# Kernel tuning notes

Measured on AMD Instinct MI355X. Metric: run time of the kernel, lower is better.

## Reference

```python
import jax, jax.numpy as jnp
import numpy as np

D_IN = 1024
D_OUT = 1024
CTX_LEN = 2048
BATCH = 4
SEQ = 2048


def setup_inputs() -> dict:
    key = jax.random.key(0)
    kx, kq, kk, kv = jax.random.split(key, 4)
    x = jax.random.normal(kx, (BATCH, SEQ, D_IN), dtype=jnp.float32)
    s = 1.0 / np.sqrt(D_IN)
    # torch nn.Linear weight is (d_out, d_in); store transposed for x @ W
    W_q = jax.random.uniform(kq, (D_IN, D_OUT), dtype=jnp.float32, minval=-s, maxval=s)
    W_k = jax.random.uniform(kk, (D_IN, D_OUT), dtype=jnp.float32, minval=-s, maxval=s)
    W_v = jax.random.uniform(kv, (D_IN, D_OUT), dtype=jnp.float32, minval=-s, maxval=s)
    return {"x": x, "W_q": W_q, "W_k": W_k, "W_v": W_v}


def reference(x, W_q, W_k, W_v):
    b, n, _ = x.shape
    d_out = W_q.shape[1]
    q = x @ W_q            # [b, n, d_out]
    k = x @ W_k
    v = x @ W_v
    scores = jnp.einsum('bqd,bkd->bqk', q, k)  # [b, n, n]
    causal = jnp.triu(jnp.ones((n, n), dtype=bool), k=1)
    scores = jnp.where(causal, -jnp.inf, scores)
    attn = jax.nn.softmax(scores / jnp.sqrt(jnp.float32(d_out)), axis=-1)
    # dropout p=0.0 -> identity
    return jnp.einsum('bqk,bkd->bqd', attn, v)
```

## Files before the change

kernel.cpp:

```cpp
#include <hip/hip_runtime.h>
#include <hip/hip_bf16.h>

#define BATCH 4
#define SEQ   2048
#define DIN   1024
#define DOUT  1024
#define N3    3072
#define MTOT  (BATCH*SEQ)

typedef __hip_bfloat16 bf16;
typedef __attribute__((ext_vector_type(8))) short bf16x8;
typedef __attribute__((ext_vector_type(4))) float f32x4;

#define MFMA(a,b,c) __builtin_amdgcn_mfma_f32_16x16x32_bf16(a,b,c,0,0,0)

union pack4 { bf16 h[4]; uint2 u2; };
union pack8 { bf16 h[8]; bf16x8 v; };

__device__ __forceinline__ void gl16(const bf16* g, bf16* l)
{
    __builtin_amdgcn_global_load_lds(
        (const __attribute__((address_space(1))) void*)g,
        (__attribute__((address_space(3))) void*)l, 16, 0, 0);
}


__global__ __launch_bounds__(256)
void k_prep(const float* __restrict__ x, const float* __restrict__ Wq,
            const float* __restrict__ Wk, const float* __restrict__ Wv,
            bf16* __restrict__ xb, bf16* __restrict__ Wt)
{
    __shared__ bf16 t[64][68];
    const int bid = blockIdx.x;
    if (bid < 8192) {
        long i = ((long)bid * 256 + threadIdx.x) * 4;
        float4 v = *(const float4*)(x + i);
        pack4 o;
        o.h[0] = __float2bfloat16(v.x);
        o.h[1] = __float2bfloat16(v.y);
        o.h[2] = __float2bfloat16(v.z);
        o.h[3] = __float2bfloat16(v.w);
        *(uint2*)(xb + i) = o.u2;
        return;
    }
    const int idx = bid - 8192;
    const int mat = idx >> 8;
    const int rem = idx & 255;
    const int k0 = (rem >> 4) * 64, n0 = (rem & 15) * 64;
    const float* W = (mat == 0) ? Wq : ((mat == 1) ? Wk : Wv);
#pragma unroll
    for (int p = 0; p < 4; ++p) {
        int kr = p * 16 + (threadIdx.x >> 4);
        int c4 = (threadIdx.x & 15) * 4;
        float4 v = *(const float4*)&W[(long)(k0 + kr) * DOUT + n0 + c4];
        t[c4 + 0][kr] = __float2bfloat16(v.x);
        t[c4 + 1][kr] = __float2bfloat16(v.y);
        t[c4 + 2][kr] = __float2bfloat16(v.z);
        t[c4 + 3][kr] = __float2bfloat16(v.w);
    }
    __syncthreads();
    bf16* O = Wt + (long)mat * DIN * DOUT;
#pragma unroll
    for (int i = 0; i < 2; ++i) {
        int l = threadIdx.x + i * 256;
        int n = l >> 3, c8 = (l & 7) * 8;
        pack8 o;
#pragma unroll
        for (int j = 0; j < 8; ++j) o.h[j] = t[n][c8 + j];
        *(bf16x8*)&O[(long)(n0 + n) * DIN + k0 + c8] = o.v;
    }
}


__device__ __forceinline__ void gemm_core(
    const bf16* __restrict__ Ab, long lda,
    const bf16* __restrict__ Bb, long ldb,
    int nk, bf16* __restrict__ As, bf16* __restrict__ Bs,
    f32x4 acc[4][4])
{
    const int tid  = threadIdx.x;
    const int lane = tid & 63;
    const int wave = tid >> 6;
    const int wm = (wave >> 1) * 64;
    const int wn = (wave & 1) * 64;
    const int r  = lane & 15;
    const int qd = lane >> 4;

    const int row0 = tid >> 3;
    const int c    = (tid & 7) ^ (row0 & 7);
    const long aoff = (long)row0 * lda + c * 8;
    const long boff = (long)row0 * ldb + c * 8;
    const long astep = 32 * lda, bstep = 32 * ldb;
    bf16* dA = &As[tid * 8];
    bf16* dB = &Bs[tid * 8];

    for (int kk = 0; kk < nk; ++kk) {
        const bf16* A = Ab + kk * 64 + aoff;
        const bf16* B = Bb + kk * 64 + boff;
#pragma unroll
        for (int i = 0; i < 4; ++i) {
            gl16(A + i * astep, dA + i * 2048);
            gl16(B + i * bstep, dB + i * 2048);
        }
        __syncthreads();
#pragma unroll
        for (int ks = 0; ks < 2; ++ks) {
            const int slot = ((ks * 4 + qd) ^ (r & 7)) * 8;
            bf16x8 af[4], bv[4];
#pragma unroll
            for (int mi = 0; mi < 4; ++mi)
                af[mi] = *(const bf16x8*)&As[(wm + mi * 16 + r) * 64 + slot];
#pragma unroll
            for (int ni = 0; ni < 4; ++ni)
                bv[ni] = *(const bf16x8*)&Bs[(wn + ni * 16 + r) * 64 + slot];
#pragma unroll
            for (int mi = 0; mi < 4; ++mi)
#pragma unroll
                for (int ni = 0; ni < 4; ++ni)
                    acc[mi][ni] = MFMA(af[mi], bv[ni], acc[mi][ni]);
        }
        __syncthreads();
    }
}


__global__ __launch_bounds__(256)
void k_gemm_qkv(const bf16* __restrict__ xb, const bf16* __restrict__ Wt,
                bf16* __restrict__ QK, bf16* __restrict__ Vt)
{
    __shared__ __align__(16) bf16 smem[17408];
    bf16* As = smem;
    bf16* Bs = smem + 8192;
    const int m0 = blockIdx.y * 128, n0 = blockIdx.x * 128;
    f32x4 acc[4][4] = {};
    gemm_core(xb + (long)m0 * DIN, DIN, Wt + (long)n0 * DIN, DIN, DIN / 64, As, Bs, acc);

    const int tid = threadIdx.x;
    const int lane = tid & 63, wave = tid >> 6;
    const int wm = (wave >> 1) * 64, wn = (wave & 1) * 64;
    const int r = lane & 15, qd = lane >> 4;

    if (n0 < 2048) {
#pragma unroll
        for (int mi = 0; mi < 4; ++mi)
#pragma unroll
            for (int ni = 0; ni < 4; ++ni)
#pragma unroll
                for (int j = 0; j < 4; ++j) {
                    int row = m0 + wm + mi * 16 + qd * 4 + j;
                    int col = n0 + wn + ni * 16 + r;
                    QK[(long)row * 2048 + col] = __float2bfloat16(acc[mi][ni][j]);
                }
    } else {
        const int ld = 136;
        bf16* T = smem;
#pragma unroll
        for (int mi = 0; mi < 4; ++mi)
#pragma unroll
            for (int ni = 0; ni < 4; ++ni) {
                pack4 p;
#pragma unroll
                for (int j = 0; j < 4; ++j) p.h[j] = __float2bfloat16(acc[mi][ni][j]);
                int d_l = wn + ni * 16 + r;
                int s_l = wm + mi * 16 + qd * 4;
                *(uint2*)&T[d_l * ld + s_l] = p.u2;
            }
        __syncthreads();
        const int n0v = n0 - 2048;
        const int bb = m0 >> 11;
        const int s0 = m0 & 2047;
        bf16* Ob = Vt + (long)bb * DOUT * SEQ + s0;
#pragma unroll
        for (int p = 0; p < 8; ++p) {
            int l = tid + p * 256;
            int d = l >> 4, s8 = (l & 15) * 8;
            bf16x8 vv = *(const bf16x8*)&T[d * ld + s8];
            *(bf16x8*)&Ob[(long)(n0v + d) * SEQ + s8] = vv;
        }
    }
}


__global__ __launch_bounds__(256, 3)
void k_gemm_scores(const bf16* __restrict__ QK, bf16* __restrict__ P,
                   float* __restrict__ rowSum)
{
    const int b = blockIdx.z, qt = blockIdx.y, kt = blockIdx.x;
    if (kt > qt) return;
    __shared__ __align__(16) bf16 As[128 * 64];
    __shared__ __align__(16) bf16 Bs[128 * 64];
    const bf16* A  = QK + (long)b * SEQ * 2048;
    const bf16* Bt = A + 1024;
    f32x4 acc[4][4] = {};
    gemm_core(A + (long)qt * 128 * 2048, 2048, Bt + (long)kt * 128 * 2048, 2048,
              DIN / 64, As, Bs, acc);

    bf16* Pb = P + (long)b * SEQ * SEQ;
    float* RS = rowSum + b * SEQ;
    const int lane = threadIdx.x & 63, wave = threadIdx.x >> 6;
    const int wm = (wave >> 1) * 64, wn = (wave & 1) * 64;
    const int r = lane & 15, qd = lane >> 4;

    float rp[4][4];
#pragma unroll
    for (int mi = 0; mi < 4; ++mi)
#pragma unroll
        for (int j = 0; j < 4; ++j) rp[mi][j] = 0.f;

#pragma unroll
    for (int mi = 0; mi < 4; ++mi)
#pragma unroll
        for (int ni = 0; ni < 4; ++ni)
#pragma unroll
            for (int j = 0; j < 4; ++j) {
                int row = qt * 128 + wm + mi * 16 + qd * 4 + j;
                int col = kt * 128 + wn + ni * 16 + r;
                float e = (col > row) ? 0.f : __expf(acc[mi][ni][j] * 0.03125f);
                rp[mi][j] += e;
                Pb[(long)row * SEQ + col] = __float2bfloat16(e);
            }
#pragma unroll
    for (int d = 1; d < 16; d <<= 1)
#pragma unroll
        for (int mi = 0; mi < 4; ++mi)
#pragma unroll
            for (int j = 0; j < 4; ++j)
                rp[mi][j] += __shfl_xor(rp[mi][j], d, 64);
    if (r == 0) {
#pragma unroll
        for (int mi = 0; mi < 4; ++mi)
#pragma unroll
            for (int j = 0; j < 4; ++j) {
                int row = qt * 128 + wm + mi * 16 + qd * 4 + j;
                atomicAdd(&RS[row], rp[mi][j]);
            }
    }
}


__global__ __launch_bounds__(256, 3)
void k_gemm_pv(const bf16* __restrict__ P, const bf16* __restrict__ Vt,
               const float* __restrict__ rowSum, float* __restrict__ O)
{
    const int b = blockIdx.z, nt = blockIdx.x;
    const int qt = (SEQ / 128 - 1) - blockIdx.y;
    __shared__ __align__(16) bf16 As[128 * 64];
    __shared__ __align__(16) bf16 Bs[128 * 64];
    const bf16* A  = P + (long)b * SEQ * SEQ + (long)qt * 128 * SEQ;
    const bf16* Bt = Vt + (long)b * DOUT * SEQ;
    const int nk = (qt + 1) * 2;
    f32x4 acc[4][4] = {};
    gemm_core(A, SEQ, Bt + (long)nt * 128 * SEQ, SEQ, nk, As, Bs, acc);

    float* Ob = O + (long)b * SEQ * DOUT;
    const float* RS = rowSum + b * SEQ;
    const int lane = threadIdx.x & 63, wave = threadIdx.x >> 6;
    const int wm = (wave >> 1) * 64, wn = (wave & 1) * 64;
    const int r = lane & 15, qd = lane >> 4;
#pragma unroll
    for (int mi = 0; mi < 4; ++mi)
#pragma unroll
        for (int j = 0; j < 4; ++j) {
            int row = qt * 128 + wm + mi * 16 + qd * 4 + j;
            float inv = 1.0f / RS[row];
#pragma unroll
            for (int ni = 0; ni < 4; ++ni) {
                int col = nt * 128 + wn + ni * 16 + r;
                Ob[(long)row * DOUT + col] = acc[mi][ni][j] * inv;
            }
        }
}


extern "C" void kernel_launch(void* const* d_in, const int* in_sizes, int n_in,
                              void* d_out, int out_size, void* d_ws, size_t ws_size,
                              hipStream_t stream)
{
    const float* x  = (const float*)d_in[0];
    const float* Wq = (const float*)d_in[1];
    const float* Wk = (const float*)d_in[2];
    const float* Wv = (const float*)d_in[3];
    float* out = (float*)d_out;

    char* ws = (char*)d_ws;
    bf16*  xb = (bf16*)(ws);
    bf16*  Wt = (bf16*)(ws + 16777216);
    bf16*  QK = (bf16*)(ws + 23068672);
    bf16*  Vt = (bf16*)(ws + 56623104);
    bf16*  P  = (bf16*)(ws + 73400320);
    float* RS = (float*)(ws + 106954752);

    hipMemsetAsync(RS, 0, BATCH * SEQ * sizeof(float), stream);
    k_prep<<<dim3(8192 + 768), 256, 0, stream>>>(x, Wq, Wk, Wv, xb, Wt);
    k_gemm_qkv<<<dim3(N3 / 128, MTOT / 128), 256, 0, stream>>>(xb, Wt, QK, Vt);
    k_gemm_scores<<<dim3(SEQ / 128, SEQ / 128, BATCH), 256, 0, stream>>>(QK, P, RS);
    k_gemm_pv<<<dim3(DOUT / 128, SEQ / 128, BATCH), 256, 0, stream>>>(P, Vt, RS, out);
}
```

Before: 225.1 us.

## Stage GEMM epilogues through LDS for coalesced stores; compact causal score grid

The QK, scores and PV epilogues now write their accumulator tiles into shared memory and then emit 16-byte coalesced global stores, replacing scattered 2-byte and 4-byte per-element stores. The PV kernel stages its fp32 output in two 64-row halves so the tile fits in the existing LDS buffer. The scores kernel launches only the 136 lower-triangular tiles per batch, recovering the (qt,kt) pair with a sqrt-based index, so no blocks launch only to exit early. The cost is extra LDS traffic and barriers in each epilogue.

```diff
diff --git a/kernel.cpp b/kernel.cpp
--- a/kernel.cpp
+++ b/kernel.cpp
@@ -139,6 +139,8 @@
     const int lane = tid & 63, wave = tid >> 6;
     const int wm = (wave >> 1) * 64, wn = (wave & 1) * 64;
     const int r = lane & 15, qd = lane >> 4;
+    const int ld = 136;
+    bf16* T = smem;
 
     if (n0 < 2048) {
 #pragma unroll
@@ -146,14 +148,18 @@
 #pragma unroll
             for (int ni = 0; ni < 4; ++ni)
 #pragma unroll
-                for (int j = 0; j < 4; ++j) {
-                    int row = m0 + wm + mi * 16 + qd * 4 + j;
-                    int col = n0 + wn + ni * 16 + r;
-                    QK[(long)row * 2048 + col] = __float2bfloat16(acc[mi][ni][j]);
-                }
+                for (int j = 0; j < 4; ++j)
+                    T[(wm + mi * 16 + qd * 4 + j) * ld + wn + ni * 16 + r] =
+                        __float2bfloat16(acc[mi][ni][j]);
+        __syncthreads();
+#pragma unroll
+        for (int i = 0; i < 8; ++i) {
+            int l = tid + i * 256;
+            int rr = l >> 4, c8 = (l & 15) * 8;
+            bf16x8 v = *(const bf16x8*)&T[rr * ld + c8];
+            *(bf16x8*)&QK[(long)(m0 + rr) * 2048 + n0 + c8] = v;
+        }
     } else {
-        const int ld = 136;
-        bf16* T = smem;
 #pragma unroll
         for (int mi = 0; mi < 4; ++mi)
 #pragma unroll
@@ -185,10 +191,16 @@
 void k_gemm_scores(const bf16* __restrict__ QK, bf16* __restrict__ P,
                    float* __restrict__ rowSum)
 {
-    const int b = blockIdx.z, qt = blockIdx.y, kt = blockIdx.x;
-    if (kt > qt) return;
-    __shared__ __align__(16) bf16 As[128 * 64];
-    __shared__ __align__(16) bf16 Bs[128 * 64];
+    const int b = blockIdx.z;
+    int i = blockIdx.x;
+    int qt = (int)((sqrtf(8.f * i + 1.f) - 1.f) * 0.5f);
+    if (qt * (qt + 1) / 2 > i) --qt;
+    else if ((qt + 1) * (qt + 2) / 2 <= i) ++qt;
+    const int kt = i - qt * (qt + 1) / 2;
+
+    __shared__ __align__(16) bf16 smem[17408];
+    bf16* As = smem;
+    bf16* Bs = smem + 8192;
     const bf16* A  = QK + (long)b * SEQ * 2048;
     const bf16* Bt = A + 1024;
     f32x4 acc[4][4] = {};
@@ -197,9 +209,12 @@
 
     bf16* Pb = P + (long)b * SEQ * SEQ;
     float* RS = rowSum + b * SEQ;
-    const int lane = threadIdx.x & 63, wave = threadIdx.x >> 6;
+    const int tid = threadIdx.x;
+    const int lane = tid & 63, wave = tid >> 6;
     const int wm = (wave >> 1) * 64, wn = (wave & 1) * 64;
     const int r = lane & 15, qd = lane >> 4;
+    const int ld = 136;
+    bf16* T = smem;
 
     float rp[4][4];
 #pragma unroll
@@ -213,12 +228,21 @@
         for (int ni = 0; ni < 4; ++ni)
 #pragma unroll
             for (int j = 0; j < 4; ++j) {
-                int row = qt * 128 + wm + mi * 16 + qd * 4 + j;
-                int col = kt * 128 + wn + ni * 16 + r;
-                float e = (col > row) ? 0.f : __expf(acc[mi][ni][j] * 0.03125f);
+                int row_l = wm + mi * 16 + qd * 4 + j;
+                int col_l = wn + ni * 16 + r;
+                float e = (kt * 128 + col_l > qt * 128 + row_l)
+                          ? 0.f : __expf(acc[mi][ni][j] * 0.03125f);
                 rp[mi][j] += e;
-                Pb[(long)row * SEQ + col] = __float2bfloat16(e);
+                T[row_l * ld + col_l] = __float2bfloat16(e);
             }
+    __syncthreads();
+#pragma unroll
+    for (int i2 = 0; i2 < 8; ++i2) {
+        int l = tid + i2 * 256;
+        int rr = l >> 4, c8 = (l & 15) * 8;
+        bf16x8 v = *(const bf16x8*)&T[rr * ld + c8];
+        *(bf16x8*)&Pb[(long)(qt * 128 + rr) * SEQ + kt * 128 + c8] = v;
+    }
 #pragma unroll
     for (int d = 1; d < 16; d <<= 1)
 #pragma unroll
@@ -244,8 +268,9 @@
 {
     const int b = blockIdx.z, nt = blockIdx.x;
     const int qt = (SEQ / 128 - 1) - blockIdx.y;
-    __shared__ __align__(16) bf16 As[128 * 64];
-    __shared__ __align__(16) bf16 Bs[128 * 64];
+    __shared__ __align__(16) bf16 smem[17408];
+    bf16* As = smem;
+    bf16* Bs = smem + 8192;
     const bf16* A  = P + (long)b * SEQ * SEQ + (long)qt * 128 * SEQ;
     const bf16* Bt = Vt + (long)b * DOUT * SEQ;
     const int nk = (qt + 1) * 2;
@@ -254,21 +279,37 @@
 
     float* Ob = O + (long)b * SEQ * DOUT;
     const float* RS = rowSum + b * SEQ;
-    const int lane = threadIdx.x & 63, wave = threadIdx.x >> 6;
-    const int wm = (wave >> 1) * 64, wn = (wave & 1) * 64;
+    const int tid = threadIdx.x;
+    const int lane = tid & 63, wave = tid >> 6;
+    const int wn = (wave & 1) * 64;
     const int r = lane & 15, qd = lane >> 4;
-#pragma unroll
-    for (int mi = 0; mi < 4; ++mi)
-#pragma unroll
-        for (int j = 0; j < 4; ++j) {
-            int row = qt * 128 + wm + mi * 16 + qd * 4 + j;
-            float inv = 1.0f / RS[row];
-#pragma unroll
-            for (int ni = 0; ni < 4; ++ni) {
-                int col = nt * 128 + wn + ni * 16 + r;
-                Ob[(long)row * DOUT + col] = acc[mi][ni][j] * inv;
-            }
-        }
+    const int ldf = 132;
+    float* T = (float*)smem;
+
+#pragma unroll
+    for (int h = 0; h < 2; ++h) {
+        if ((wave >> 1) == h) {
+#pragma unroll
+            for (int mi = 0; mi < 4; ++mi)
+#pragma unroll
+                for (int j = 0; j < 4; ++j) {
+                    int row_l = mi * 16 + qd * 4 + j;
+                    float inv = 1.0f / RS[qt * 128 + h * 64 + row_l];
+#pragma unroll
+                    for (int ni = 0; ni < 4; ++ni)
+                        T[row_l * ldf + wn + ni * 16 + r] = acc[mi][ni][j] * inv;
+                }
+        }
+        __syncthreads();
+#pragma unroll
+        for (int i = 0; i < 8; ++i) {
+            int l = tid + i * 256;
+            int rr = l >> 5, c4 = (l & 31) * 4;
+            float4 v = *(const float4*)&T[rr * ldf + c4];
+            *(float4*)&Ob[(long)(qt * 128 + h * 64 + rr) * DOUT + nt * 128 + c4] = v;
+        }
+        __syncthreads();
+    }
 }
 
 
@@ -293,6 +334,6 @@
     hipMemsetAsync(RS, 0, BATCH * SEQ * sizeof(float), stream);
     k_prep<<<dim3(8192 + 768), 256, 0, stream>>>(x, Wq, Wk, Wv, xb, Wt);
     k_gemm_qkv<<<dim3(N3 / 128, MTOT / 128), 256, 0, stream>>>(xb, Wt, QK, Vt);
-    k_gemm_scores<<<dim3(SEQ / 128, SEQ / 128, BATCH), 256, 0, stream>>>(QK, P, RS);
+    k_gemm_scores<<<dim3(136, 1, BATCH), 256, 0, stream>>>(QK, P, RS);
     k_gemm_pv<<<dim3(DOUT / 128, SEQ / 128, BATCH), 256, 0, stream>>>(P, Vt, RS, out);
 }
```

Measured after the change: 232.9 us. 3.5% more time.

## Double-buffer LDS in attention GEMMs, compact causal grid, stage QK stores via LDS

Applied to the files above, without the earlier changes.

Adds a double-buffered GEMM core that prefetches the next K-slice into a second LDS buffer while MFMAs run on the current one. The scores and PV kernels use it, with occupancy hints lowered to 2 blocks because LDS per block doubles. The scores launch now covers only the 136 lower-triangular tiles per batch, decoding (qt, kt) with a sqrt, so no blocks launch just to exit. The QKV epilogue stages Q/K tiles through LDS so global writes are 16-byte vectors instead of scattered 2-byte stores.

```diff
diff --git a/kernel.cpp b/kernel.cpp
--- a/kernel.cpp
+++ b/kernel.cpp
@@ -124,6 +124,72 @@
 }
 
 
+__device__ __forceinline__ void gemm_core_db(
+    const bf16* __restrict__ Ab, long lda,
+    const bf16* __restrict__ Bb, long ldb,
+    int nk, bf16* __restrict__ As, bf16* __restrict__ Bs,
+    f32x4 acc[4][4])
+{
+    const int tid  = threadIdx.x;
+    const int lane = tid & 63;
+    const int wave = tid >> 6;
+    const int wm = (wave >> 1) * 64;
+    const int wn = (wave & 1) * 64;
+    const int r  = lane & 15;
+    const int qd = lane >> 4;
+
+    const int row0 = tid >> 3;
+    const int c    = (tid & 7) ^ (row0 & 7);
+    const long aoff = (long)row0 * lda + c * 8;
+    const long boff = (long)row0 * ldb + c * 8;
+    const long astep = 32 * lda, bstep = 32 * ldb;
+
+    {
+        const bf16* A = Ab + aoff;
+        const bf16* B = Bb + boff;
+        bf16* dA = &As[tid * 8];
+        bf16* dB = &Bs[tid * 8];
+#pragma unroll
+        for (int i = 0; i < 4; ++i) {
+            gl16(A + i * astep, dA + i * 2048);
+            gl16(B + i * bstep, dB + i * 2048);
+        }
+    }
+    for (int kk = 0; kk < nk; ++kk) {
+        __syncthreads();
+        const int cur = (kk & 1) * 8192;
+        if (kk + 1 < nk) {
+            const int nxt = 8192 - cur;
+            const bf16* A = Ab + (kk + 1) * 64 + aoff;
+            const bf16* B = Bb + (kk + 1) * 64 + boff;
+            bf16* dA = &As[nxt + tid * 8];
+            bf16* dB = &Bs[nxt + tid * 8];
+#pragma unroll
+            for (int i = 0; i < 4; ++i) {
+                gl16(A + i * astep, dA + i * 2048);
+                gl16(B + i * bstep, dB + i * 2048);
+            }
+        }
+#pragma unroll
+        for (int ks = 0; ks < 2; ++ks) {
+            const int slot = ((ks * 4 + qd) ^ (r & 7)) * 8;
+            bf16x8 af[4], bv[4];
+#pragma unroll
+            for (int mi = 0; mi < 4; ++mi)
+                af[mi] = *(const bf16x8*)&As[cur + (wm + mi * 16 + r) * 64 + slot];
+#pragma unroll
+            for (int ni = 0; ni < 4; ++ni)
+                bv[ni] = *(const bf16x8*)&Bs[cur + (wn + ni * 16 + r) * 64 + slot];
+#pragma unroll
+            for (int mi = 0; mi < 4; ++mi)
+#pragma unroll
+                for (int ni = 0; ni < 4; ++ni)
+                    acc[mi][ni] = MFMA(af[mi], bv[ni], acc[mi][ni]);
+        }
+    }
+}
+
+
 __global__ __launch_bounds__(256)
 void k_gemm_qkv(const bf16* __restrict__ xb, const bf16* __restrict__ Wt,
                 bf16* __restrict__ QK, bf16* __restrict__ Vt)
@@ -139,6 +205,8 @@
     const int lane = tid & 63, wave = tid >> 6;
     const int wm = (wave >> 1) * 64, wn = (wave & 1) * 64;
     const int r = lane & 15, qd = lane >> 4;
+    const int ld = 136;
+    bf16* T = smem;
 
     if (n0 < 2048) {
 #pragma unroll
@@ -146,14 +214,18 @@
 #pragma unroll
             for (int ni = 0; ni < 4; ++ni)
 #pragma unroll
-                for (int j = 0; j < 4; ++j) {
-                    int row = m0 + wm + mi * 16 + qd * 4 + j;
-                    int col = n0 + wn + ni * 16 + r;
-                    QK[(long)row * 2048 + col] = __float2bfloat16(acc[mi][ni][j]);
-                }
+                for (int j = 0; j < 4; ++j)
+                    T[(wm + mi * 16 + qd * 4 + j) * ld + wn + ni * 16 + r] =
+                        __float2bfloat16(acc[mi][ni][j]);
+        __syncthreads();
+#pragma unroll
+        for (int i = 0; i < 8; ++i) {
+            int l = tid + i * 256;
+            int rr = l >> 4, c8 = (l & 15) * 8;
+            bf16x8 v = *(const bf16x8*)&T[rr * ld + c8];
+            *(bf16x8*)&QK[(long)(m0 + rr) * 2048 + n0 + c8] = v;
+        }
     } else {
-        const int ld = 136;
-        bf16* T = smem;
 #pragma unroll
         for (int mi = 0; mi < 4; ++mi)
 #pragma unroll
@@ -181,19 +253,24 @@
 }
 
 
-__global__ __launch_bounds__(256, 3)
+__global__ __launch_bounds__(256, 2)
 void k_gemm_scores(const bf16* __restrict__ QK, bf16* __restrict__ P,
                    float* __restrict__ rowSum)
 {
-    const int b = blockIdx.z, qt = blockIdx.y, kt = blockIdx.x;
-    if (kt > qt) return;
-    __shared__ __align__(16) bf16 As[128 * 64];
-    __shared__ __align__(16) bf16 Bs[128 * 64];
+    const int b = blockIdx.z;
+    int i = blockIdx.x;
+    int qt = (int)((sqrtf(8.f * i + 1.f) - 1.f) * 0.5f);
+    if (qt * (qt + 1) / 2 > i) --qt;
+    else if ((qt + 1) * (qt + 2) / 2 <= i) ++qt;
+    const int kt = i - qt * (qt + 1) / 2;
+
+    __shared__ __align__(16) bf16 As[2 * 8192];
+    __shared__ __align__(16) bf16 Bs[2 * 8192];
     const bf16* A  = QK + (long)b * SEQ * 2048;
     const bf16* Bt = A + 1024;
     f32x4 acc[4][4] = {};
-    gemm_core(A + (long)qt * 128 * 2048, 2048, Bt + (long)kt * 128 * 2048, 2048,
-              DIN / 64, As, Bs, acc);
+    gemm_core_db(A + (long)qt * 128 * 2048, 2048, Bt + (long)kt * 128 * 2048, 2048,
+                 DIN / 64, As, Bs, acc);
 
     bf16* Pb = P + (long)b * SEQ * SEQ;
     float* RS = rowSum + b * SEQ;
@@ -238,19 +315,19 @@
 }
 
 
-__global__ __launch_bounds__(256, 3)
+__global__ __launch_bounds__(256, 2)
 void k_gemm_pv(const bf16* __restrict__ P, const bf16* __restrict__ Vt,
                const float* __restrict__ rowSum, float* __restrict__ O)
 {
     const int b = blockIdx.z, nt = blockIdx.x;
     const int qt = (SEQ / 128 - 1) - blockIdx.y;
-    __shared__ __align__(16) bf16 As[128 * 64];
-    __shared__ __align__(16) bf16 Bs[128 * 64];
+    __shared__ __align__(16) bf16 As[2 * 8192];
+    __shared__ __align__(16) bf16 Bs[2 * 8192];
     const bf16* A  = P + (long)b * SEQ * SEQ + (long)qt * 128 * SEQ;
     const bf16* Bt = Vt + (long)b * DOUT * SEQ;
     const int nk = (qt + 1) * 2;
     f32x4 acc[4][4] = {};
-    gemm_core(A, SEQ, Bt + (long)nt * 128 * SEQ, SEQ, nk, As, Bs, acc);
+    gemm_core_db(A, SEQ, Bt + (long)nt * 128 * SEQ, SEQ, nk, As, Bs, acc);
 
     float* Ob = O + (long)b * SEQ * DOUT;
     const float* RS = rowSum + b * SEQ;
@@ -293,6 +370,6 @@
     hipMemsetAsync(RS, 0, BATCH * SEQ * sizeof(float), stream);
     k_prep<<<dim3(8192 + 768), 256, 0, stream>>>(x, Wq, Wk, Wv, xb, Wt);
     k_gemm_qkv<<<dim3(N3 / 128, MTOT / 128), 256, 0, stream>>>(xb, Wt, QK, Vt);
-    k_gemm_scores<<<dim3(SEQ / 128, SEQ / 128, BATCH), 256, 0, stream>>>(QK, P, RS);
+    k_gemm_scores<<<dim3(136, 1, BATCH), 256, 0, stream>>>(QK, P, RS);
     k_gemm_pv<<<dim3(DOUT / 128, SEQ / 128, BATCH), 256, 0, stream>>>(P, Vt, RS, out);
 }
```

Result: slower. 237.7 us (+5.6%).
